# Performance work log

Measured on AMD Instinct MI355X. Metric: run time of the kernel, lower is better.

The kernel has to match this reference:

```python
import jax, jax.numpy as jnp
import numpy as np

N_NODES = 50000
N_GRAPHS = 250
NODES_PER_GRAPH = 200
EDGES_PER_GRAPH = 3200  # avg degree 16
F_IN = 128
EMB = 128
HID = 128
VOCAB = 1000
N_REL = 8


def setup_inputs() -> dict:
    key = jax.random.key(0)
    ks = jax.random.split(key, 16)

    # message: col 0 = discrete token id (stored as float), col 1 = continuous value
    disc = jax.random.randint(ks[0], (N_GRAPHS,), 0, VOCAB).astype(jnp.float32)
    cont = jax.random.normal(ks[1], (N_GRAPHS,), dtype=jnp.float32)
    message = jnp.stack([disc, cont], axis=1)  # [B, 2]

    x = jax.random.normal(ks[2], (N_NODES, F_IN), dtype=jnp.float32)

    # within-graph edges: local indices + per-graph node offset
    offs = (jnp.arange(N_GRAPHS, dtype=jnp.int64) * NODES_PER_GRAPH)[:, None]
    src = (jax.random.randint(ks[3], (N_GRAPHS, EDGES_PER_GRAPH), 0, NODES_PER_GRAPH) + offs).reshape(-1)
    dst = (jax.random.randint(ks[4], (N_GRAPHS, EDGES_PER_GRAPH), 0, NODES_PER_GRAPH) + offs).reshape(-1)
    edge_index = jnp.stack([src, dst], axis=0).astype(jnp.int64)  # [2, E]
    edge_type = jax.random.randint(ks[5], (N_GRAPHS * EDGES_PER_GRAPH,), 0, N_REL).astype(jnp.int64)

    batch = jnp.repeat(jnp.arange(N_GRAPHS, dtype=jnp.int64), NODES_PER_GRAPH)  # [N]

    s = 0.05
    W1 = jax.random.normal(ks[6], (N_REL, F_IN, EMB), dtype=jnp.float32) * s
    root1 = jax.random.normal(ks[7], (F_IN, EMB), dtype=jnp.float32) * s
    b1 = jnp.zeros((EMB,), dtype=jnp.float32)
    W2 = jax.random.normal(ks[8], (N_REL, EMB, EMB), dtype=jnp.float32) * s
    root2 = jax.random.normal(ks[9], (EMB, EMB), dtype=jnp.float32) * s
    b2 = jnp.zeros((EMB,), dtype=jnp.float32)
    embed_table = jax.random.normal(ks[10], (VOCAB, EMB), dtype=jnp.float32) * s
    cont_w = jax.random.normal(ks[11], (1, EMB), dtype=jnp.float32) * s
    cont_b = jnp.zeros((EMB,), dtype=jnp.float32)
    msg_w = jax.random.normal(ks[12], (2 * EMB, HID), dtype=jnp.float32) * s
    msg_b = jnp.zeros((HID,), dtype=jnp.float32)

    return {
        "message": message, "x": x, "edge_index": edge_index, "edge_type": edge_type,
        "batch": batch, "max_nodes": NODES_PER_GRAPH,
        "W1": W1, "root1": root1, "b1": b1, "W2": W2, "root2": root2, "b2": b2,
        "embed_table": embed_table, "cont_w": cont_w, "cont_b": cont_b,
        "msg_w": msg_w, "msg_b": msg_b,
    }


def _rgcn_conv(h, src, dst, edge_type, W, root, b, n_nodes, n_rel):
    # per-node per-relation transform, then gather per edge: avoids [E,F,F] weight gather
    hW = jnp.einsum('nf,rfo->nro', h, W)          # [N, R, O]
    msg = hW[src, edge_type]                       # [E, O]
    # mean aggregation per (dst, relation) as in PyG RGCNConv(aggr='mean')
    key_dr = dst * n_rel + edge_type
    cnt = jax.ops.segment_sum(jnp.ones_like(edge_type, dtype=h.dtype), key_dr,
                              num_segments=n_nodes * n_rel)
    norm = 1.0 / jnp.maximum(cnt[key_dr], 1.0)     # [E]
    agg = jax.ops.segment_sum(msg * norm[:, None], dst, num_segments=n_nodes)  # [N, O]
    return agg + h @ root + b


def reference(message, x, edge_index, edge_type, batch, max_nodes,
              W1, root1, b1, W2, root2, b2,
              embed_table, cont_w, cont_b, msg_w, msg_b):
    n_nodes = x.shape[0]
    n_rel = W1.shape[0]
    n_graphs = message.shape[0]
    src, dst = edge_index[0], edge_index[1]

    # --- RGCN node embeddings (2 layers, ReLU between) ---
    h = _rgcn_conv(x, src, dst, edge_type, W1, root1, b1, n_nodes, n_rel)
    h = jax.nn.relu(h)
    node_emb = _rgcn_conv(h, src, dst, edge_type, W2, root2, b2, n_nodes, n_rel)  # [N, EMB]

    # --- message representation ---
    disc_tok = message[:, 0].astype(jnp.int32)
    disc_emb = embed_table[disc_tok]                                   # [B, EMB]
    cont_emb = jax.nn.relu(message[:, 1:2] @ cont_w + cont_b)          # [B, EMB]
    combined = jnp.concatenate([disc_emb, cont_emb], axis=1)           # [B, 2*EMB]
    message_repr = jax.nn.relu(combined @ msg_w + msg_b)               # [B, HID]

    # --- per-node dot score against its graph's message, padded per graph ---
    scores = jnp.einsum('ne,ne->n', node_emb, message_repr[batch])     # [N]
    counts = jax.ops.segment_sum(jnp.ones((n_nodes,), dtype=jnp.int32), batch,
                                 num_segments=n_graphs)
    start = jnp.cumsum(counts) - counts                                # exclusive cumsum
    pos = jnp.arange(n_nodes) - start[batch]                           # slot within graph
    logits = jnp.full((n_graphs, max_nodes), -jnp.inf, dtype=scores.dtype)
    logits = logits.at[batch, pos].set(scores)
    return logits
```

## Files before the change

### kernel.cpp

```cpp
#include <hip/hip_runtime.h>
#include <stdint.h>

#define G_   250
#define P_   200
#define EPG  3200
#define E_   800000
#define F_   128
#define R_   8
#define HROW 136
#define NKEY (R_ * P_)

typedef _Float16 f16x8 __attribute__((ext_vector_type(8)));
typedef _Float16 f16x4 __attribute__((ext_vector_type(4)));
typedef float    f32x4 __attribute__((ext_vector_type(4)));
typedef float    f32x16 __attribute__((ext_vector_type(16)));

__global__ __launch_bounds__(256) void k_wstage(const float* __restrict__ W1, const float* __restrict__ root1,
                                                const float* __restrict__ W2, const float* __restrict__ root2,
                                                _Float16* __restrict__ wf) {
  int t = blockIdx.x * 256 + threadIdx.x;
  int n = t & 127;
  int k = (t >> 7) & 127;
  int rl_ = t >> 14;
  int r = rl_ % 9, l = rl_ / 9;
  const float* Wl = (l == 0) ? W1 : W2;
  const float* rt = (l == 0) ? root1 : root2;
  float v = (r < 8) ? Wl[(r * F_ + k) * F_ + n] : rt[k * F_ + n];
  int lane = (n & 31) | (((k >> 3) & 1) << 5);
  int j = k & 7, kt = k >> 4, ntj = n >> 5;
  wf[((((l * 9 + r) * 8 + kt) * 4 + ntj) * 64 + lane) * 8 + j] = (_Float16)v;
}

__global__ __launch_bounds__(512, 2) void k_main(
    const float* __restrict__ x, const int* __restrict__ ei, const int* __restrict__ et,
    const _Float16* __restrict__ wf, const float* __restrict__ b1, const float* __restrict__ b2,
    const float* __restrict__ message, const float* __restrict__ embed,
    const float* __restrict__ cw, const float* __restrict__ cb,
    const float* __restrict__ mw, const float* __restrict__ mb,
    float* __restrict__ out) {
  __shared__ __attribute__((aligned(16))) _Float16 hbuf0[P_ * HROW];
  __shared__ __attribute__((aligned(16))) _Float16 hbuf1[P_ * HROW];
  __shared__ unsigned short csrS[EPG];
  __shared__ int offsS[NKEY + 1];
  __shared__ float msgS[F_ + 1];

  int g = blockIdx.x, tid = threadIdx.x;
  int lane = tid & 63, wave = tid >> 6;
  int m32 = lane & 31, kh = lane >> 5;

  int*   Sint = (int*)hbuf1;
  int*   cnt  = Sint;
  int*   cur  = Sint + 1600;
  int*   eRec = Sint + 3200;
  float* comb = (float*)(Sint + 6400);
  float* red  = (float*)(Sint + 6656);

  for (int i = tid; i < P_ * 32; i += 512) {
    int row = i >> 5, c4 = i & 31;
    const float4 v = ((const float4*)x)[(g * P_ + row) * 32 + c4];
    f16x4 pk = { (_Float16)v.x, (_Float16)v.y, (_Float16)v.z, (_Float16)v.w };
    *((f16x4*)&hbuf0[row * HROW + c4 * 4]) = pk;
  }
  for (int i = tid; i < NKEY; i += 512) { cnt[i] = 0; cur[i] = 0; }
  if (tid < F_) {
    int tok = (int)message[g * 2];
    float cont = message[g * 2 + 1];
    comb[tid] = embed[tok * F_ + tid];
    float ce = cont * cw[tid] + cb[tid];
    comb[F_ + tid] = ce > 0.0f ? ce : 0.0f;
  }
  __syncthreads();

  int base = g * EPG, nbase = g * P_;
  if (wave < 6) {
    for (int e = wave * 64 + lane; e < EPG; e += 384) {
      int s = ei[base + e] - nbase;
      int d = ei[E_ + base + e] - nbase;
      int r = et[base + e];
      eRec[e] = s | (d << 8) | (r << 16);
      atomicAdd(&cnt[r * P_ + d], 1);
    }
  } else {
    int col = tid & 127;
    float acc = 0.0f;
#pragma unroll 16
    for (int k2 = 0; k2 < 256; k2++) acc += comb[k2] * mw[k2 * F_ + col];
    red[col] = acc;
  }
  __syncthreads();

  if (wave == 0) {
    int4 vv[8];
    int osum = 0;
    if (lane < 50) {
      const int4* cp = (const int4*)(cnt + lane * 32);
#pragma unroll
      for (int i = 0; i < 8; i++) { vv[i] = cp[i]; osum += vv[i].x + vv[i].y + vv[i].z + vv[i].w; }
    }
    int incl = osum;
#pragma unroll
    for (int d = 1; d < 64; d <<= 1) {
      int t2 = __shfl_up(incl, d, 64);
      if (lane >= d) incl += t2;
    }
    int run = incl - osum;
    if (lane < 50) {
#pragma unroll
      for (int i = 0; i < 8; i++) {
        offsS[lane * 32 + i * 4 + 0] = run; run += vv[i].x;
        offsS[lane * 32 + i * 4 + 1] = run; run += vv[i].y;
        offsS[lane * 32 + i * 4 + 2] = run; run += vv[i].z;
        offsS[lane * 32 + i * 4 + 3] = run; run += vv[i].w;
      }
    }
    if (lane == 0) offsS[NKEY] = EPG;
  } else if (wave == 1) {
    float m0 = mb[lane] + red[lane];
    float m1 = mb[lane + 64] + red[lane + 64];
    m0 = m0 > 0.0f ? m0 : 0.0f;
    m1 = m1 > 0.0f ? m1 : 0.0f;
    msgS[lane] = m0; msgS[lane + 64] = m1;
    float p = m0 * b2[lane] + m1 * b2[lane + 64];
#pragma unroll
    for (int d = 32; d > 0; d >>= 1) p += __shfl_xor(p, d, 64);
    if (lane == 0) msgS[F_] = p;
  }
  __syncthreads();

  for (int e = tid; e < EPG; e += 512) {
    int rec = eRec[e];
    int s = rec & 255, d = (rec >> 8) & 255, r = rec >> 16;
    int key = r * P_ + d;
    int pos = atomicAdd(&cur[key], 1);
    csrS[offsS[key] + pos] = (unsigned short)s;
  }
  __syncthreads();

  int jobBase = wave * 25;
  bool rowAct = (m32 < 25);
  int myD = jobBase + m32;
  int ck = kh * 8;

  for (int l = 0; l < 2; l++) {
    const _Float16* Ap = (l == 0) ? hbuf0 : hbuf1;
    f32x16 acc[4];
#pragma unroll
    for (int nt = 0; nt < 4; nt++)
#pragma unroll
      for (int i = 0; i < 16; i++) acc[nt][i] = 0.0f;
    const _Float16* wl = wf + l * (9 * 8 * 4 * 64 * 8);
    for (int r = 0; r < 9; r++) {
      const _Float16* wr = wl + r * (8 * 4 * 64 * 8);
      f16x8 Bn[8];
#pragma unroll
      for (int kt = 0; kt < 8; kt++)
        Bn[kt] = *((const f16x8*)(wr + ((kt * 4 + 0) * 64 + lane) * 8));
      f16x8 a[8];
      if (r < 8) {
        int o = 0, n = 0;
        if (rowAct) { int key = r * P_ + myD; o = offsS[key]; n = offsS[key + 1] - o; }
        f16x8 z = {0, 0, 0, 0, 0, 0, 0, 0};
#pragma unroll
        for (int kt = 0; kt < 8; kt++) a[kt] = z;
        int sNext = (n > 0) ? (int)csrS[o] : 0;
        for (int t = 0; t < n; t++) {
          int sc = sNext;
          if (t + 1 < n) sNext = (int)csrS[o + t + 1];
          const _Float16* hp = &Ap[sc * HROW + ck];
#pragma unroll
          for (int kt = 0; kt < 8; kt++) a[kt] += *((const f16x8*)(hp + kt * 16));
        }
        float nf = (n > 0) ? 1.0f / (float)n : 0.0f;
        _Float16 nh = (_Float16)nf;
#pragma unroll
        for (int kt = 0; kt < 8; kt++) a[kt] *= nh;
      } else {
        int rowA = jobBase + (rowAct ? m32 : 24);
        const _Float16* hp = &Ap[rowA * HROW + ck];
#pragma unroll
        for (int kt = 0; kt < 8; kt++) a[kt] = *((const f16x8*)(hp + kt * 16));
      }
#pragma unroll
      for (int nt = 0; nt < 4; nt++) {
        f16x8 Bx[8];
        if (nt < 3) {
#pragma unroll
          for (int kt = 0; kt < 8; kt++)
            Bx[kt] = *((const f16x8*)(wr + ((kt * 4 + nt + 1) * 64 + lane) * 8));
        }
#pragma unroll
        for (int kt = 0; kt < 8; kt++)
          acc[nt] = __builtin_amdgcn_mfma_f32_32x32x16_f16(a[kt], Bn[kt], acc[nt], 0, 0, 0);
        if (nt < 3) {
#pragma unroll
          for (int kt = 0; kt < 8; kt++) Bn[kt] = Bx[kt];
        }
      }
    }
    if (l == 0) {
      __syncthreads();
#pragma unroll
      for (int nt = 0; nt < 4; nt++) {
        int col = nt * 32 + m32;
        float bias = b1[col];
#pragma unroll
        for (int reg = 0; reg < 16; reg++) {
          int row = (reg & 3) + 8 * (reg >> 2) + 4 * kh;
          if (row < 25) {
            float v = acc[nt][reg] + bias;
            v = v > 0.0f ? v : 0.0f;
            hbuf1[(jobBase + row) * HROW + col] = (_Float16)v;
          }
        }
      }
      __syncthreads();
    } else {
      float db2 = msgS[F_];
#pragma unroll
      for (int reg = 0; reg < 16; reg++) {
        int row = (reg & 3) + 8 * (reg >> 2) + 4 * kh;
        float p = 0.0f;
#pragma unroll
        for (int nt = 0; nt < 4; nt++)
          p += acc[nt][reg] * msgS[nt * 32 + m32];
        p += __shfl_xor(p, 16, 32);
        p += __shfl_xor(p, 8, 32);
        p += __shfl_xor(p, 4, 32);
        p += __shfl_xor(p, 2, 32);
        p += __shfl_xor(p, 1, 32);
        if (m32 == 0 && row < 25)
          out[g * P_ + jobBase + row] = p + db2;
      }
    }
  }
}

extern "C" void kernel_launch(void* const* d_in, const int* in_sizes, int n_in,
                              void* d_out, int out_size, void* d_ws, size_t ws_size,
                              hipStream_t stream) {
  const float* message = (const float*)d_in[0];
  const float* x       = (const float*)d_in[1];
  const int*   ei      = (const int*)d_in[2];
  const int*   et      = (const int*)d_in[3];
  const float* W1      = (const float*)d_in[6];
  const float* root1   = (const float*)d_in[7];
  const float* b1      = (const float*)d_in[8];
  const float* W2      = (const float*)d_in[9];
  const float* root2   = (const float*)d_in[10];
  const float* b2      = (const float*)d_in[11];
  const float* embed   = (const float*)d_in[12];
  const float* cw      = (const float*)d_in[13];
  const float* cb      = (const float*)d_in[14];
  const float* mw      = (const float*)d_in[15];
  const float* mb      = (const float*)d_in[16];

  _Float16* wfrag = (_Float16*)d_ws;
  float*    out   = (float*)d_out;

  hipLaunchKernelGGL(k_wstage, dim3(1152), dim3(256), 0, stream, W1, root1, W2, root2, wfrag);
  hipLaunchKernelGGL(k_main, dim3(G_), dim3(512), 0, stream, x, ei, et, wfrag, b1, b2,
                     message, embed, cw, cb, mw, mb, out);
}
```

Baseline: 195.7 us.

## Stage per-relation weight tiles in shared memory and pair neighbor gathers

Each relation's fp16 weight block is now loaded cooperatively by all 512 threads into a shared-memory staging buffer, and the MFMA loop reads B fragments from LDS instead of each wave loading the full block from global memory. The neighbor aggregation loop is unrolled by two so two source rows are fetched in flight per iteration. Launch bounds drop from 2 to 1 blocks per CU to make room for the extra 32KB of LDS. This adds two block-wide barriers per relation and may reduce occupancy.

```diff
diff --git a/kernel.cpp b/kernel.cpp
--- a/kernel.cpp
+++ b/kernel.cpp
@@ -9,6 +9,7 @@
 #define R_   8
 #define HROW 136
 #define NKEY (R_ * P_)
+#define BSTG (8 * 4 * 64 * 8)
 
 typedef _Float16 f16x8 __attribute__((ext_vector_type(8)));
 typedef _Float16 f16x4 __attribute__((ext_vector_type(4)));
@@ -31,7 +32,7 @@
   wf[((((l * 9 + r) * 8 + kt) * 4 + ntj) * 64 + lane) * 8 + j] = (_Float16)v;
 }
 
-__global__ __launch_bounds__(512, 2) void k_main(
+__global__ __launch_bounds__(512, 1) void k_main(
     const float* __restrict__ x, const int* __restrict__ ei, const int* __restrict__ et,
     const _Float16* __restrict__ wf, const float* __restrict__ b1, const float* __restrict__ b2,
     const float* __restrict__ message, const float* __restrict__ embed,
@@ -40,6 +41,7 @@
     float* __restrict__ out) {
   __shared__ __attribute__((aligned(16))) _Float16 hbuf0[P_ * HROW];
   __shared__ __attribute__((aligned(16))) _Float16 hbuf1[P_ * HROW];
+  __shared__ __attribute__((aligned(16))) _Float16 Bstage[BSTG];
   __shared__ unsigned short csrS[EPG];
   __shared__ int offsS[NKEY + 1];
   __shared__ float msgS[F_ + 1];
@@ -148,13 +150,13 @@
     for (int nt = 0; nt < 4; nt++)
 #pragma unroll
       for (int i = 0; i < 16; i++) acc[nt][i] = 0.0f;
-    const _Float16* wl = wf + l * (9 * 8 * 4 * 64 * 8);
+    const _Float16* wl = wf + l * (9 * BSTG);
     for (int r = 0; r < 9; r++) {
-      const _Float16* wr = wl + r * (8 * 4 * 64 * 8);
-      f16x8 Bn[8];
-#pragma unroll
-      for (int kt = 0; kt < 8; kt++)
-        Bn[kt] = *((const f16x8*)(wr + ((kt * 4 + 0) * 64 + lane) * 8));
+      const _Float16* wr = wl + r * BSTG;
+      f16x8 st[4];
+#pragma unroll
+      for (int i = 0; i < 4; i++)
+        st[i] = *((const f16x8*)(wr + i * 4096 + tid * 8));
       f16x8 a[8];
       if (r < 8) {
         int o = 0, n = 0;
@@ -162,13 +164,25 @@
         f16x8 z = {0, 0, 0, 0, 0, 0, 0, 0};
 #pragma unroll
         for (int kt = 0; kt < 8; kt++) a[kt] = z;
-        int sNext = (n > 0) ? (int)csrS[o] : 0;
-        for (int t = 0; t < n; t++) {
-          int sc = sNext;
-          if (t + 1 < n) sNext = (int)csrS[o + t + 1];
-          const _Float16* hp = &Ap[sc * HROW + ck];
-#pragma unroll
-          for (int kt = 0; kt < 8; kt++) a[kt] += *((const f16x8*)(hp + kt * 16));
+        int t = 0;
+        for (; t + 2 <= n; t += 2) {
+          int s0 = (int)csrS[o + t];
+          int s1 = (int)csrS[o + t + 1];
+          const _Float16* hp0 = &Ap[s0 * HROW + ck];
+          const _Float16* hp1 = &Ap[s1 * HROW + ck];
+          f16x8 u0[8], u1[8];
+#pragma unroll
+          for (int kt = 0; kt < 8; kt++) u0[kt] = *((const f16x8*)(hp0 + kt * 16));
+#pragma unroll
+          for (int kt = 0; kt < 8; kt++) u1[kt] = *((const f16x8*)(hp1 + kt * 16));
+#pragma unroll
+          for (int kt = 0; kt < 8; kt++) a[kt] += u0[kt] + u1[kt];
+        }
+        if (t < n) {
+          int s0 = (int)csrS[o + t];
+          const _Float16* hp0 = &Ap[s0 * HROW + ck];
+#pragma unroll
+          for (int kt = 0; kt < 8; kt++) a[kt] += *((const f16x8*)(hp0 + kt * 16));
         }
         float nf = (n > 0) ? 1.0f / (float)n : 0.0f;
         _Float16 nh = (_Float16)nf;
@@ -181,24 +195,20 @@
         for (int kt = 0; kt < 8; kt++) a[kt] = *((const f16x8*)(hp + kt * 16));
       }
 #pragma unroll
+      for (int i = 0; i < 4; i++)
+        *((f16x8*)(Bstage + i * 4096 + tid * 8)) = st[i];
+      __syncthreads();
+#pragma unroll
       for (int nt = 0; nt < 4; nt++) {
-        f16x8 Bx[8];
-        if (nt < 3) {
-#pragma unroll
-          for (int kt = 0; kt < 8; kt++)
-            Bx[kt] = *((const f16x8*)(wr + ((kt * 4 + nt + 1) * 64 + lane) * 8));
-        }
-#pragma unroll
-        for (int kt = 0; kt < 8; kt++)
-          acc[nt] = __builtin_amdgcn_mfma_f32_32x32x16_f16(a[kt], Bn[kt], acc[nt], 0, 0, 0);
-        if (nt < 3) {
-#pragma unroll
-          for (int kt = 0; kt < 8; kt++) Bn[kt] = Bx[kt];
-        }
-      }
+#pragma unroll
+        for (int kt = 0; kt < 8; kt++) {
+          f16x8 b = *((const f16x8*)&Bstage[((kt * 4 + nt) * 64 + lane) * 8]);
+          acc[nt] = __builtin_amdgcn_mfma_f32_32x32x16_f16(a[kt], b, acc[nt], 0, 0, 0);
+        }
+      }
+      __syncthreads();
     }
     if (l == 0) {
-      __syncthreads();
 #pragma unroll
       for (int nt = 0; nt < 4; nt++) {
         int col = nt * 32 + m32;
```

Result: faster. 176.5 us (-9.8%).
